# Optimization experiments

Hardware: AMD Instinct MI355X
Metric: run time of the kernel (lower is better)

Reference implementation:

```python
import jax, jax.numpy as jnp
import numpy as np

GATE_DECAY = 3.0

def setup_inputs() -> dict:
    key = jax.random.key(0)
    ks = jax.random.split(key, 4)
    B, S, D, I = 8, 2048, 512, 2048
    x = jax.random.normal(ks[0], (B, S, D), dtype=jnp.float32)
    # kaiming normal fan_in, linear gain: std = 1/sqrt(fan_in)
    Wa = jax.random.normal(ks[1], (I, D), dtype=jnp.float32) / np.sqrt(D)
    Wi = jax.random.normal(ks[2], (I, D), dtype=jnp.float32) / np.sqrt(D)
    ba = jnp.zeros((I,), dtype=jnp.float32)
    bi = jnp.zeros((I,), dtype=jnp.float32)
    lo, hi = np.log(0.9 / 0.1), np.log(0.999 / 0.001)  # logit(0.9), logit(0.999)
    gate = jax.random.uniform(ks[3], (I,), dtype=jnp.float32, minval=lo, maxval=hi)
    return {"x": x, "Wa": Wa, "ba": ba, "Wi": Wi, "bi": bi, "gate": gate}

def reference(x, Wa, ba, Wi, bi, gate):
    # Precompute both projections for all timesteps as large GEMMs.
    pa = jnp.einsum('bsd,id->bsi', x, Wa) + ba   # [B,S,I]
    pi = jnp.einsum('bsd,id->bsi', x, Wi) + bi   # [B,S,I]
    reset_gate = jax.nn.sigmoid(pa)
    input_gate = jax.nn.sigmoid(pi)
    alpha = jax.nn.sigmoid(gate)                  # [I]
    adaptive_alpha = alpha / (GATE_DECAY ** reset_gate)          # [B,S,I]
    drive = jnp.sqrt(1.0 - adaptive_alpha ** 2) * (input_gate * pi)
    B, S, I = pa.shape

    def step(h, ac):
        a, c = ac
        h = a * h + c
        return h, h

    h0 = jnp.zeros((B, I), dtype=x.dtype)
    # scan over time: move S to leading axis
    _, ys = jax.lax.scan(step, h0, (adaptive_alpha.transpose(1, 0, 2), drive.transpose(1, 0, 2)))
    return ys.transpose(1, 0, 2)  # [B,S,I]
```

## Files before the change

kernel.cpp:

```cpp
#include <hip/hip_runtime.h>


#define LOG2_3 1.5849625007211562f

typedef _Float16 f16x8 __attribute__((ext_vector_type(8)));
typedef _Float16 f16x4 __attribute__((ext_vector_type(4)));
typedef _Float16 f16x2 __attribute__((ext_vector_type(2)));
typedef float f32x4 __attribute__((ext_vector_type(4)));

__device__ __forceinline__ float sigmoid_fast(float v) {
  return __fdividef(1.0f, 1.0f + __expf(-v));
}

__device__ __forceinline__ void async_copy16(void* lds, const void* gp) {
  __builtin_amdgcn_global_load_lds((__attribute__((address_space(1))) void*)gp,
                                   (__attribute__((address_space(3))) void*)lds,
                                   16, 0, 0);
}

__global__ __launch_bounds__(256) void cvt_all(const float* __restrict__ x,
                                               const float* __restrict__ Wa,
                                               const float* __restrict__ Wi,
                                               _Float16* __restrict__ xh,
                                               _Float16* __restrict__ wh) {
  int idx = blockIdx.x * 256 + threadIdx.x;
  const float* src;
  _Float16* dst;
  int off, doff;
  if (idx < 2097152) {
    src = x; dst = xh; off = idx; doff = idx;
  } else if (idx < 2097152 + 262144) {
    src = Wa; dst = wh; off = idx - 2097152;
    doff = off + ((off >> 7) << 7);
  } else {
    src = Wi; dst = wh; off = idx - 2359296;
    doff = off + ((off >> 7) << 7) + 128;
  }
  float4 v = ((const float4*)src)[off];
  f16x4 h;
  h[0] = (_Float16)v.x;
  h[1] = (_Float16)v.y;
  h[2] = (_Float16)v.z;
  h[3] = (_Float16)v.w;
  ((f16x4*)dst)[doff] = h;
}

__device__ __forceinline__ void gate_ac(float pa, float pi, float alpha, float& a, float& c) {
  float rg = sigmoid_fast(pa);
  a = alpha * exp2f(-LOG2_3 * rg);
  float ig = sigmoid_fast(pi);
  float m = fmaxf(1.0f - a * a, 1e-8f);
  c = (m * __frsqrt_rn(m)) * (ig * pi);
}

__global__ __launch_bounds__(512) void gemm_ac(const _Float16* __restrict__ Ah,
                                               const _Float16* __restrict__ Wh,
                                               const float* __restrict__ ba,
                                               const float* __restrict__ bi,
                                               const float* __restrict__ gate,
                                               _Float16* __restrict__ AC) {
  constexpr int K = 512;
  __shared__ __align__(16) _Float16 smem[32768];
  const int t = threadIdx.x;
  const int bx = blockIdx.x;
  const int by = blockIdx.y;
  const int mBase = by * 256;
  const int nBase = bx * 256;
  const int r = t >> 2;
  const int p = t & 3;
  const int lsw = p ^ ((r >> 1) & 3);
  const _Float16* gA0 = Ah + (size_t)(mBase + r) * K + lsw * 8;
  const _Float16* gB0 = Wh + (size_t)(nBase + r) * K + lsw * 8;
  const int ldst = r * 32 + p * 8;

  const int lane = t & 63;
  const int wave = t >> 6;
  const int wm = (wave & 1) * 128;
  const int wn = (wave >> 1) * 64;
  const int lrow = lane & 15;
  const int quad = lane >> 4;
  const int xq = quad ^ ((lrow >> 1) & 3);

  f32x4 acc[8][4];
#pragma unroll
  for (int i = 0; i < 8; ++i)
#pragma unroll
    for (int j = 0; j < 4; ++j)
      acc[i][j] = (f32x4)0.0f;

  _Float16* b0 = smem;
  _Float16* b1 = smem + 16384;

  auto STAGE = [&](int tt, _Float16* bb) {
    const int ko = tt * 32;
    async_copy16(bb + ldst, gA0 + ko);
    async_copy16(bb + 4096 + ldst, gA0 + (size_t)128 * K + ko);
    async_copy16(bb + 8192 + ldst, gB0 + ko);
    async_copy16(bb + 12288 + ldst, gB0 + (size_t)128 * K + ko);
  };

  STAGE(0, b0);
  __syncthreads();

#pragma unroll
  for (int kt = 0; kt < 16; ++kt) {
    _Float16* cur = (kt & 1) ? b1 : b0;
    _Float16* nxt = (kt & 1) ? b0 : b1;
    if (kt < 15) STAGE(kt + 1, nxt);
    f16x8 af[8], bf[4];
#pragma unroll
    for (int i = 0; i < 8; ++i)
      af[i] = *(const f16x8*)(cur + (wm + i * 16 + lrow) * 32 + xq * 8);
#pragma unroll
    for (int j = 0; j < 4; ++j)
      bf[j] = *(const f16x8*)(cur + 8192 + (wn + j * 16 + lrow) * 32 + xq * 8);
#pragma unroll
    for (int i = 0; i < 8; ++i)
#pragma unroll
      for (int j = 0; j < 4; ++j)
        acc[i][j] = __builtin_amdgcn_mfma_f32_16x16x32_f16(af[i], bf[j], acc[i][j], 0, 0, 0);
    __syncthreads();
  }

  const int odd = lane & 1;
  float bias[4], alpha[4];
#pragma unroll
  for (int j = 0; j < 4; ++j) {
    const int n = nBase + wn + j * 16 + lrow;
    bias[j] = odd ? bi[n >> 1] : ba[n >> 1];
    alpha[j] = sigmoid_fast(gate[n >> 1]);
  }

  _Float16* pp = AC + (((size_t)by * 16 + bx) << 16) + wave * 8192 + lane * 4;
#pragma unroll
  for (int i = 0; i < 8; ++i)
#pragma unroll
    for (int j = 0; j < 4; ++j) {
      f16x4 st;
#pragma unroll
      for (int rr = 0; rr < 4; ++rr) {
        float own = acc[i][j][rr] + bias[j];
        float par = __shfl_xor(own, 1);
        float pa = odd ? par : own;
        float pi = odd ? own : par;
        float a, c;
        gate_ac(pa, pi, alpha[j], a, c);
        st[rr] = (_Float16)(odd ? c : a);
      }
      *(f16x4*)(pp + i * 1024 + j * 256) = st;
    }
}

__global__ __launch_bounds__(256) void gate_agg(const _Float16* __restrict__ AC,
                                                float2* __restrict__ agg) {
  const int tt = blockIdx.x * 256 + threadIdx.x;
  const int ch = blockIdx.y;
  const int b = blockIdx.z;
  const int n = tt * 2;
  const int bx = n >> 8;
  const int nl = n & 255;
  const int wn_idx = nl >> 6;
  const int j = (nl >> 4) & 3;
  const int lrow = nl & 15;
  const int by = b * 8 + (ch >> 3);
  const int c8 = ch & 7;
  const int wm_bit = c8 >> 2;
  const _Float16* base = AC + (((size_t)by * 16 + bx) << 16) +
                         (wm_bit + 2 * wn_idx) * 8192 + j * 256 + lrow * 4;
  f16x8 v[8];
#pragma unroll
  for (int u = 0; u < 8; ++u) {
    const int i = (c8 * 2 + (u >> 2)) & 7;
    v[u] = *(const f16x8*)(base + i * 1024 + (u & 3) * 64);
  }
  float A = 1.0f, H = 0.0f;
#pragma unroll
  for (int u = 0; u < 8; ++u)
#pragma unroll
    for (int rr = 0; rr < 4; ++rr) {
      float a = (float)v[u][rr];
      float c = (float)v[u][4 + rr];
      A *= a;
      H = fmaf(a, H, c);
    }
  agg[((size_t)(b * 64 + ch)) * 2048 + tt] = make_float2(A, H);
}

__global__ __launch_bounds__(64) void scan_pass2(const float2* __restrict__ agg,
                                                 float* __restrict__ carry) {
  const int i = blockIdx.x * 64 + threadIdx.x;
  const int b = blockIdx.y;
  float h = 0.0f;
  for (int c8 = 0; c8 < 8; ++c8) {
    float2 aH[8];
#pragma unroll
    for (int u = 0; u < 8; ++u)
      aH[u] = agg[((size_t)(b * 64 + c8 * 8 + u)) * 2048 + i];
#pragma unroll
    for (int u = 0; u < 8; ++u) {
      carry[((size_t)(b * 64 + c8 * 8 + u)) * 2048 + i] = h;
      h = fmaf(aH[u].x, h, aH[u].y);
    }
  }
}

__global__ __launch_bounds__(256) void scan_out(const _Float16* __restrict__ AC,
                                                const float* __restrict__ carry,
                                                float* __restrict__ out) {
  const int tt = blockIdx.x * 256 + threadIdx.x;
  const int ch = blockIdx.y;
  const int b = blockIdx.z;
  float h = carry[((size_t)(b * 64 + ch)) * 2048 + tt];
  const int n = tt * 2;
  const int bx = n >> 8;
  const int nl = n & 255;
  const int wn_idx = nl >> 6;
  const int j = (nl >> 4) & 3;
  const int lrow = nl & 15;
  const int by = b * 8 + (ch >> 3);
  const int c8 = ch & 7;
  const int wm_bit = c8 >> 2;
  const _Float16* base = AC + (((size_t)by * 16 + bx) << 16) +
                         (wm_bit + 2 * wn_idx) * 8192 + j * 256 + lrow * 4;
  f16x8 v[8];
#pragma unroll
  for (int u = 0; u < 8; ++u) {
    const int i = (c8 * 2 + (u >> 2)) & 7;
    v[u] = *(const f16x8*)(base + i * 1024 + (u & 3) * 64);
  }
  float* orow = out + ((size_t)(b * 2048 + ch * 32)) * 2048 + tt;
#pragma unroll
  for (int u = 0; u < 8; ++u)
#pragma unroll
    for (int rr = 0; rr < 4; ++rr) {
      h = fmaf((float)v[u][rr], h, (float)v[u][4 + rr]);
      __builtin_nontemporal_store(h, orow);
      orow += 2048;
    }
}

extern "C" void kernel_launch(void* const* d_in, const int* in_sizes, int n_in,
                              void* d_out, int out_size, void* d_ws, size_t ws_size,
                              hipStream_t stream) {
  const float* x = (const float*)d_in[0];
  const float* Wa = (const float*)d_in[1];
  const float* ba = (const float*)d_in[2];
  const float* Wi = (const float*)d_in[3];
  const float* bi = (const float*)d_in[4];
  const float* gate = (const float*)d_in[5];
  float* out = (float*)d_out;

  char* ws = (char*)d_ws;
  _Float16* xh = (_Float16*)ws;
  _Float16* wh = (_Float16*)(ws + 16777216);
  const size_t MN2 = (size_t)16384 * 4096;
  _Float16* AC = (_Float16*)(ws + 20971520);
  float2* agg = (float2*)(ws + 20971520 + MN2 * 2);
  float* carry = (float*)(ws + 20971520 + MN2 * 2 + 8388608);

  cvt_all<<<10240, 256, 0, stream>>>(x, Wa, Wi, xh, wh);
  gemm_ac<<<dim3(16, 64), 512, 0, stream>>>(xh, wh, ba, bi, gate, AC);
  gate_agg<<<dim3(8, 64, 8), 256, 0, stream>>>(AC, agg);
  scan_pass2<<<dim3(32, 8), 64, 0, stream>>>(agg, carry);
  scan_out<<<dim3(8, 64, 8), 256, 0, stream>>>(AC, carry, out);
}
```

Measured before the change: 389.1 us.

## Group Wa/Wi rows in 16-row blocks to drop epilogue lane shuffles

The interleaving of Wa and Wi rows in the fp16 weight buffer changes from alternating single rows to alternating 16-row blocks. A thread's MFMA accumulators now hold matching pa and pi values in adjacent j tiles, so the GEMM epilogue no longer needs __shfl_xor or the odd/even selects. Each lane now computes the gate once per element pair instead of twice redundantly. The a/c outputs are stored as separate f16x4 tiles, and the scan kernels switch from 16-byte to two 8-byte loads to match the new AC layout, which may cost some load efficiency there.

```diff
diff --git a/kernel.cpp b/kernel.cpp
--- a/kernel.cpp
+++ b/kernel.cpp
@@ -31,10 +31,12 @@
     src = x; dst = xh; off = idx; doff = idx;
   } else if (idx < 2097152 + 262144) {
     src = Wa; dst = wh; off = idx - 2097152;
-    doff = off + ((off >> 7) << 7);
+    const int i = off >> 7, k4 = off & 127;
+    doff = (((((i >> 4) << 5) | (i & 15))) << 7) | k4;
   } else {
     src = Wi; dst = wh; off = idx - 2359296;
-    doff = off + ((off >> 7) << 7) + 128;
+    const int i = off >> 7, k4 = off & 127;
+    doff = (((((i >> 4) << 5) | 16 | (i & 15))) << 7) | k4;
   }
   float4 v = ((const float4*)src)[off];
   f16x4 h;
@@ -67,19 +69,19 @@
   const int mBase = by * 256;
   const int nBase = bx * 256;
   const int r = t >> 2;
-  const int p = t & 3;
-  const int lsw = p ^ ((r >> 1) & 3);
+  const int p4 = t & 3;
+  const int lsw = p4 ^ ((r >> 1) & 3);
   const _Float16* gA0 = Ah + (size_t)(mBase + r) * K + lsw * 8;
   const _Float16* gB0 = Wh + (size_t)(nBase + r) * K + lsw * 8;
-  const int ldst = r * 32 + p * 8;
+  const int ldst = r * 32 + p4 * 8;
 
   const int lane = t & 63;
   const int wave = t >> 6;
   const int wm = (wave & 1) * 128;
-  const int wn = (wave >> 1) * 64;
   const int lrow = lane & 15;
   const int quad = lane >> 4;
   const int xq = quad ^ ((lrow >> 1) & 3);
+  const int wn = (wave >> 1) * 64;
 
   f32x4 acc[8][4];
 #pragma unroll
@@ -122,32 +124,33 @@
     __syncthreads();
   }
 
-  const int odd = lane & 1;
-  float bias[4], alpha[4];
-#pragma unroll
-  for (int j = 0; j < 4; ++j) {
-    const int n = nBase + wn + j * 16 + lrow;
-    bias[j] = odd ? bi[n >> 1] : ba[n >> 1];
-    alpha[j] = sigmoid_fast(gate[n >> 1]);
+  const int G = bx * 4 + (wave >> 1);
+  float bav[2], biv[2], alphav[2];
+#pragma unroll
+  for (int p = 0; p < 2; ++p) {
+    const int u = G * 32 + p * 16 + lrow;
+    bav[p] = ba[u];
+    biv[p] = bi[u];
+    alphav[p] = sigmoid_fast(gate[u]);
   }
 
   _Float16* pp = AC + (((size_t)by * 16 + bx) << 16) + wave * 8192 + lane * 4;
 #pragma unroll
   for (int i = 0; i < 8; ++i)
 #pragma unroll
-    for (int j = 0; j < 4; ++j) {
-      f16x4 st;
+    for (int p = 0; p < 2; ++p) {
+      f16x4 sa, sc;
 #pragma unroll
       for (int rr = 0; rr < 4; ++rr) {
-        float own = acc[i][j][rr] + bias[j];
-        float par = __shfl_xor(own, 1);
-        float pa = odd ? par : own;
-        float pi = odd ? own : par;
+        float pa = acc[i][2 * p][rr] + bav[p];
+        float pi = acc[i][2 * p + 1][rr] + biv[p];
         float a, c;
-        gate_ac(pa, pi, alpha[j], a, c);
-        st[rr] = (_Float16)(odd ? c : a);
+        gate_ac(pa, pi, alphav[p], a, c);
+        sa[rr] = (_Float16)a;
+        sc[rr] = (_Float16)c;
       }
-      *(f16x4*)(pp + i * 1024 + j * 256) = st;
+      *(f16x4*)(pp + i * 1024 + (2 * p) * 256) = sa;
+      *(f16x4*)(pp + i * 1024 + (2 * p + 1) * 256) = sc;
     }
 }
 
@@ -156,33 +159,31 @@
   const int tt = blockIdx.x * 256 + threadIdx.x;
   const int ch = blockIdx.y;
   const int b = blockIdx.z;
-  const int n = tt * 2;
-  const int bx = n >> 8;
-  const int nl = n & 255;
-  const int wn_idx = nl >> 6;
-  const int j = (nl >> 4) & 3;
-  const int lrow = nl & 15;
+  const int G = tt >> 5;
+  const int bx = G >> 2;
+  const int wn_idx = G & 3;
+  const int within = tt & 31;
+  const int p = within >> 4;
+  const int lrow = within & 15;
   const int by = b * 8 + (ch >> 3);
   const int c8 = ch & 7;
   const int wm_bit = c8 >> 2;
   const _Float16* base = AC + (((size_t)by * 16 + bx) << 16) +
-                         (wm_bit + 2 * wn_idx) * 8192 + j * 256 + lrow * 4;
-  f16x8 v[8];
+                         (wm_bit + 2 * wn_idx) * 8192 + (2 * p) * 256 + lrow * 4;
+  float A = 1.0f, H = 0.0f;
 #pragma unroll
   for (int u = 0; u < 8; ++u) {
-    const int i = (c8 * 2 + (u >> 2)) & 7;
-    v[u] = *(const f16x8*)(base + i * 1024 + (u & 3) * 64);
-  }
-  float A = 1.0f, H = 0.0f;
-#pragma unroll
-  for (int u = 0; u < 8; ++u)
+    const int i = ((c8 & 3) << 1) + (u >> 2);
+    const _Float16* q = base + i * 1024 + (u & 3) * 64;
+    f16x4 va = *(const f16x4*)q;
+    f16x4 vc = *(const f16x4*)(q + 256);
 #pragma unroll
     for (int rr = 0; rr < 4; ++rr) {
-      float a = (float)v[u][rr];
-      float c = (float)v[u][4 + rr];
+      float a = (float)va[rr];
       A *= a;
-      H = fmaf(a, H, c);
-    }
+      H = fmaf(a, H, (float)vc[rr]);
+    }
+  }
   agg[((size_t)(b * 64 + ch)) * 2048 + tt] = make_float2(A, H);
 }
 
@@ -211,32 +212,31 @@
   const int ch = blockIdx.y;
   const int b = blockIdx.z;
   float h = carry[((size_t)(b * 64 + ch)) * 2048 + tt];
-  const int n = tt * 2;
-  const int bx = n >> 8;
-  const int nl = n & 255;
-  const int wn_idx = nl >> 6;
-  const int j = (nl >> 4) & 3;
-  const int lrow = nl & 15;
+  const int G = tt >> 5;
+  const int bx = G >> 2;
+  const int wn_idx = G & 3;
+  const int within = tt & 31;
+  const int p = within >> 4;
+  const int lrow = within & 15;
   const int by = b * 8 + (ch >> 3);
   const int c8 = ch & 7;
   const int wm_bit = c8 >> 2;
   const _Float16* base = AC + (((size_t)by * 16 + bx) << 16) +
-                         (wm_bit + 2 * wn_idx) * 8192 + j * 256 + lrow * 4;
-  f16x8 v[8];
+                         (wm_bit + 2 * wn_idx) * 8192 + (2 * p) * 256 + lrow * 4;
+  float* orow = out + ((size_t)(b * 2048 + ch * 32)) * 2048 + tt;
 #pragma unroll
   for (int u = 0; u < 8; ++u) {
-    const int i = (c8 * 2 + (u >> 2)) & 7;
-    v[u] = *(const f16x8*)(base + i * 1024 + (u & 3) * 64);
-  }
-  float* orow = out + ((size_t)(b * 2048 + ch * 32)) * 2048 + tt;
-#pragma unroll
-  for (int u = 0; u < 8; ++u)
+    const int i = ((c8 & 3) << 1) + (u >> 2);
+    const _Float16* q = base + i * 1024 + (u & 3) * 64;
+    f16x4 va = *(const f16x4*)q;
+    f16x4 vc = *(const f16x4*)(q + 256);
 #pragma unroll
     for (int rr = 0; rr < 4; ++rr) {
-      h = fmaf((float)v[u][rr], h, (float)v[u][4 + rr]);
+      h = fmaf((float)va[rr], h, (float)vc[rr]);
       __builtin_nontemporal_store(h, orow);
       orow += 2048;
     }
+  }
 }
 
 extern "C" void kernel_launch(void* const* d_in, const int* in_sizes, int n_in,
```

Measured after the change: 332.5 us. 1.17x faster.
